# Kernel tuning notes

Measured on AMD Instinct MI355X. Metric: run time of the kernel, lower is better.

The kernel has to match this reference:

```python
import jax, jax.numpy as jnp
import numpy as np
import math

B, N, D, L, H, FF, T = 8, 256, 384, 6, 8, 1536, 4
Dh = D // H  # 48, divisible by 6 for 3D rotary
N_M1 = T + 1 + 2 * N  # learn tokens + state + hand + head
S = 2 * N_M1


def rotary_pe_3d(x, coords):
    # x: [B,H,S,Dh], coords: [B,S,3]. Split head dim into 3 axis chunks,
    # apply standard RoPE per axis using the continuous coordinate as position.
    dh = x.shape[-1]
    d = dh // 3
    half = d // 2
    inv_freq = 1.0 / (10000.0 ** (jnp.arange(half, dtype=x.dtype) / half))
    outs = []
    for a in range(3):
        xa = x[..., a * d:(a + 1) * d]
        ang = coords[..., a][:, None, :, None] * inv_freq  # [B,1,S,half]
        c, s = jnp.cos(ang), jnp.sin(ang)
        x1, x2 = xa[..., :half], xa[..., half:]
        outs.append(jnp.concatenate([x1 * c - x2 * s, x1 * s + x2 * c], axis=-1))
    return jnp.concatenate(outs, axis=-1)


def layernorm(x, g, b):
    m = jnp.mean(x, axis=-1, keepdims=True)
    v = jnp.var(x, axis=-1, keepdims=True)
    return (x - m) * jax.lax.rsqrt(v + 1e-5) * g + b


def transformer_layer(src, coords_src, mask, Wq, bq, Wk, bk, Wv, bv, Wo, bo, W1, b1, W2, b2, g1, be1, g2, be2):
    Bsz, Ss, _ = src.shape
    q = jnp.einsum('bsd,od->bso', src, Wq) + bq
    k = jnp.einsum('bsd,od->bso', src, Wk) + bk
    v = jnp.einsum('bsd,od->bso', src, Wv) + bv
    q = q.reshape(Bsz, Ss, H, Dh).transpose(0, 2, 1, 3)
    k = k.reshape(Bsz, Ss, H, Dh).transpose(0, 2, 1, 3)
    v = v.reshape(Bsz, Ss, H, Dh).transpose(0, 2, 1, 3)
    q = rotary_pe_3d(q, coords_src)
    k = rotary_pe_3d(k, coords_src)
    scores = jnp.einsum('bhqd,bhkd->bhqk', q, k) / math.sqrt(Dh)
    scores = jnp.where(mask[None, None, :, :], -jnp.inf, scores)
    attn = jnp.einsum('bhqk,bhkd->bhqd', jax.nn.softmax(scores, axis=-1), v)
    attn = attn.transpose(0, 2, 1, 3).reshape(Bsz, Ss, D)
    attn = jnp.einsum('bsd,od->bso', attn, Wo) + bo
    src2 = layernorm(src + attn, g1, be1)
    ff = jnp.einsum('bsf,of->bso', jax.nn.gelu(jnp.einsum('bsd,fd->bsf', src2, W1) + b1, approximate=False), W2) + b2
    return layernorm(src2 + ff, g2, be2)


def setup_inputs() -> dict:
    key = jax.random.key(0)
    ks = jax.random.split(key, 32)
    rnd = lambda i, shape, scale=1.0: (jax.random.normal(ks[i], shape, dtype=jnp.float32) * scale)
    inp = {
        'hand_token_t': rnd(0, (B, N, D)),
        'head_token_t': rnd(1, (B, N, D)),
        'hand_token_m1': rnd(2, (B, N, D)),
        'head_token_m1': rnd(3, (B, N, D)),
        'coords_hand_t': rnd(4, (B, N, 3)),
        'coords_head_t': rnd(5, (B, N, 3)),
        'coords_hand_m1': rnd(6, (B, N, 3)),
        'coords_head_m1': rnd(7, (B, N, 3)),
        'state_t': rnd(8, (B, D)),
        'state_m1': rnd(9, (B, D)),
        'trans_head_t': rnd(10, (B, 3)),
        'trans_head_m1': rnd(11, (B, 3)),
        'tokens_m1': rnd(12, (1, T, D), 0.02),
        'tokens_t': rnd(13, (1, T, D), 0.02),
        'Wq': rnd(14, (L, D, D), 0.02), 'bq': jnp.zeros((L, D), jnp.float32),
        'Wk': rnd(15, (L, D, D), 0.02), 'bk': jnp.zeros((L, D), jnp.float32),
        'Wv': rnd(16, (L, D, D), 0.02), 'bv': jnp.zeros((L, D), jnp.float32),
        'Wo': rnd(17, (L, D, D), 0.02), 'bo': jnp.zeros((L, D), jnp.float32),
        'W1': rnd(18, (L, FF, D), 0.02), 'b1': jnp.zeros((L, FF), jnp.float32),
        'W2': rnd(19, (L, D, FF), 0.02), 'b2': jnp.zeros((L, D), jnp.float32),
        'g1': jnp.ones((L, D), jnp.float32), 'be1': jnp.zeros((L, D), jnp.float32),
        'g2': jnp.ones((L, D), jnp.float32), 'be2': jnp.zeros((L, D), jnp.float32),
    }
    return inp


def reference(hand_token_t, head_token_t, hand_token_m1, head_token_m1,
              coords_hand_t, coords_head_t, coords_hand_m1, coords_head_m1,
              state_t, state_m1, trans_head_t, trans_head_m1,
              tokens_m1, tokens_t, Wq, bq, Wk, bk, Wv, bv, Wo, bo,
              W1, b1, W2, b2, g1, be1, g2, be2):
    # Build token sequence: [state_m1, hand_m1, head_m1, learn_m1, state_t, hand_t, head_t, learn_t]
    tok_m1 = jnp.broadcast_to(tokens_m1, (B, T, D))
    tok_t = jnp.broadcast_to(tokens_t, (B, T, D))
    coord_m1 = jnp.broadcast_to(trans_head_m1[:, None, :], (B, T, 3))
    coord_t = jnp.broadcast_to(trans_head_t[:, None, :], (B, T, 3))
    src = jnp.concatenate([
        state_m1[:, None, :], hand_token_m1, head_token_m1, tok_m1,
        state_t[:, None, :], hand_token_t, head_token_t, tok_t], axis=1)
    coords_src = jnp.concatenate([
        trans_head_m1[:, None, :], coords_hand_m1, coords_head_m1, coord_m1,
        trans_head_t[:, None, :], coords_hand_t, coords_head_t, coord_t], axis=1)
    # block-causal mask: m1 block cannot attend to t block
    mask = jnp.zeros((S, S), dtype=bool).at[:N_M1, N_M1:].set(True)
    for i in range(L):
        src = transformer_layer(src, coords_src, mask,
                                Wq[i], bq[i], Wk[i], bk[i], Wv[i], bv[i], Wo[i], bo[i],
                                W1[i], b1[i], W2[i], b2[i], g1[i], be1[i], g2[i], be2[i])
    return src[:, -T:, :]
```

## Files before the change

### kernel.cpp

```cpp
#include <hip/hip_runtime.h>
#include <hip/hip_bf16.h>
#include <math.h>

#define BB 8
#define NN 256
#define DD 384
#define LL 6
#define HH 8
#define FFD 1536
#define TT 4
#define DH 48
#define NM1 517
#define SS 1034
#define SSP 1088
#define MROWS (BB*SS)
#define NQKV 1152
#define QSCALE2 (0.14433756729740643f * 1.4426950408889634f)

typedef unsigned short u16;
typedef unsigned int u32;
typedef short bf8 __attribute__((ext_vector_type(8)));
typedef float f32x4 __attribute__((ext_vector_type(4)));

__device__ __forceinline__ u16 f2bf(float f) {
  __hip_bfloat16 h = __float2bfloat16(f);
  return *reinterpret_cast<u16*>(&h);
}
__device__ __forceinline__ float bf2f(u16 u) {
  __hip_bfloat16 h;
  *reinterpret_cast<u16*>(&h) = u;
  return __bfloat162float(h);
}
__device__ __forceinline__ float max3f(float a, float b, float c) {
  return fmaxf(fmaxf(a, b), c);
}
__device__ __forceinline__ void async16(void* lds, const void* g) {
  __builtin_amdgcn_global_load_lds(
      (const __attribute__((address_space(1))) unsigned int*)g,
      (__attribute__((address_space(3))) unsigned int*)lds, 16, 0, 0);
}

__global__ void build_src(const float* __restrict__ hand_t, const float* __restrict__ head_t,
                          const float* __restrict__ hand_m1, const float* __restrict__ head_m1,
                          const float* __restrict__ state_t, const float* __restrict__ state_m1,
                          const float* __restrict__ tok_m1, const float* __restrict__ tok_t,
                          float* __restrict__ src, u16* __restrict__ srcb) {
  int idx = blockIdx.x * 256 + threadIdx.x;
  if (idx >= BB * SS * DD) return;
  int d = idx % DD;
  int bs = idx / DD;
  int s = bs % SS;
  int b = bs / SS;
  float val;
  if (s == 0)               val = state_m1[b * DD + d];
  else if (s <= NN)         val = hand_m1[((size_t)(b * NN + (s - 1))) * DD + d];
  else if (s <= 2 * NN)     val = head_m1[((size_t)(b * NN + (s - 1 - NN))) * DD + d];
  else if (s <= 2 * NN + TT) val = tok_m1[(s - (2 * NN + 1)) * DD + d];
  else if (s == NM1)        val = state_t[b * DD + d];
  else if (s <= NM1 + NN)   val = hand_t[((size_t)(b * NN + (s - NM1 - 1))) * DD + d];
  else if (s <= NM1 + 2 * NN) val = head_t[((size_t)(b * NN + (s - NM1 - 1 - NN))) * DD + d];
  else                      val = tok_t[(s - (NM1 + 2 * NN + 1)) * DD + d];
  src[idx] = val;
  srcb[idx] = f2bf(val);
}

__global__ void build_coords(const float* __restrict__ c_hand_t, const float* __restrict__ c_head_t,
                             const float* __restrict__ c_hand_m1, const float* __restrict__ c_head_m1,
                             const float* __restrict__ tr_t, const float* __restrict__ tr_m1,
                             float* __restrict__ coords) {
  int idx = blockIdx.x * 256 + threadIdx.x;
  if (idx >= BB * SS * 3) return;
  int a = idx % 3;
  int bs = idx / 3;
  int s = bs % SS;
  int b = bs / SS;
  float val;
  if (s == 0)               val = tr_m1[b * 3 + a];
  else if (s <= NN)         val = c_hand_m1[(b * NN + (s - 1)) * 3 + a];
  else if (s <= 2 * NN)     val = c_head_m1[(b * NN + (s - 1 - NN)) * 3 + a];
  else if (s <= 2 * NN + TT) val = tr_m1[b * 3 + a];
  else if (s == NM1)        val = tr_t[b * 3 + a];
  else if (s <= NM1 + NN)   val = c_hand_t[(b * NN + (s - NM1 - 1)) * 3 + a];
  else if (s <= NM1 + 2 * NN) val = c_head_t[(b * NN + (s - NM1 - 1 - NN)) * 3 + a];
  else                      val = tr_t[b * 3 + a];
  coords[idx] = val;
}

__global__ void build_trig(const float* __restrict__ coords, float2* __restrict__ trig) {
  int idx = blockIdx.x * 256 + threadIdx.x;
  if (idx >= BB * SS * 24) return;
  int i = idx & 7;
  int axis = (idx >> 3) % 3;
  int bs = idx / 24;
  float cv = coords[bs * 3 + axis];
  float inv = expf(-(float)i * 1.1512925464970229f);
  float ang = cv * inv;
  trig[idx] = make_float2(cosf(ang), sinf(ang));
}

__global__ void cvt_bf(const float* __restrict__ in, u16* __restrict__ out, int n4) {
  int idx = blockIdx.x * 256 + threadIdx.x;
  if (idx >= n4) return;
  float4 v = reinterpret_cast<const float4*>(in)[idx];
  short4 o;
  o.x = (short)f2bf(v.x); o.y = (short)f2bf(v.y);
  o.z = (short)f2bf(v.z); o.w = (short)f2bf(v.w);
  reinterpret_cast<short4*>(out)[idx] = o;
}

__global__ void pack_qkv(const float* __restrict__ Wq, const float* __restrict__ Wk,
                         const float* __restrict__ Wv, u16* __restrict__ wqkv) {
  int idx = blockIdx.x * 256 + threadIdx.x;
  const int TOTAL = LL * NQKV * 96;
  if (idx >= TOTAL) return;
  int k4 = idx % 96;
  int n = (idx / 96) % NQKV;
  int l = idx / (96 * NQKV);
  int sel = n / 384, nn = n - sel * 384;
  const float* W = (sel == 0) ? Wq : ((sel == 1) ? Wk : Wv);
  float4 v = *reinterpret_cast<const float4*>(W + ((size_t)l * 384 + nn) * 384 + k4 * 4);
  short4 o;
  o.x = (short)f2bf(v.x); o.y = (short)f2bf(v.y);
  o.z = (short)f2bf(v.z); o.w = (short)f2bf(v.w);
  *reinterpret_cast<short4*>(wqkv + ((size_t)(l * NQKV + n) * 384 + k4 * 4)) = o;
}

__global__ void pack_bqkv(const float* __restrict__ bq, const float* __restrict__ bk,
                          const float* __restrict__ bv, float* __restrict__ bqkv) {
  int idx = blockIdx.x * 256 + threadIdx.x;
  if (idx >= LL * NQKV) return;
  int n = idx % NQKV, l = idx / NQKV;
  int sel = n / 384, nn = n - sel * 384;
  const float* Bp = (sel == 0) ? bq : ((sel == 1) ? bk : bv);
  bqkv[idx] = Bp[l * 384 + nn];
}

__global__ void pad_vt(u16* __restrict__ vt) {
  int idx = blockIdx.x * 256 + threadIdx.x;
  const int PADW = SSP - SS;
  if (idx >= 64 * DH * PADW) return;
  int c = idx % PADW;
  int rd = idx / PADW;
  vt[(size_t)rd * SSP + SS + c] = 0;
}

__global__ void pad_qk(u16* __restrict__ qh, u16* __restrict__ kh) {
  int idx = blockIdx.x * 256 + threadIdx.x;
  if (idx >= 64 * SS * 16) return;
  int c = idx & 15;
  int row = idx >> 4;
  qh[(size_t)row * 64 + 48 + c] = 0;
  kh[(size_t)row * 64 + 48 + c] = 0;
}

template <int EPI, int OUT>
__global__ __launch_bounds__(512) void gemm_as(
    const u16* __restrict__ Ab, const u16* __restrict__ Wb,
    const float* __restrict__ bias, const float2* __restrict__ trig,
    const float* __restrict__ Rf,
    float* __restrict__ Cf, u16* __restrict__ Cb,
    u16* __restrict__ Ck, u16* __restrict__ Cv,
    int M, int N, int K) {
  constexpr int BUFSZ = 24576;
  __shared__ __align__(16) char sm[2 * BUFSZ];
  const int tid = threadIdx.x;

  const int nxt = N >> 6;
  const int Mt = (M + 127) >> 7;
  const int gL = blockIdx.x;
  const int x8 = gL & 7, jj = gL >> 3;
  const int mt_ = x8 * 9 + jj / nxt;
  if (mt_ >= Mt) return;
  const int bm = mt_ << 7, bn = (jj % nxt) << 6;

  const int lid = tid & 63, w = tid >> 6;
  const int wm = w >> 1, wn = w & 1;
  const int l15 = lid & 15, lg = lid >> 4;
  const int lr = lid >> 3, lu = lid & 7;
  const int swz = lu ^ lr;
  f32x4 acc[2][2] = {};

  auto stage = [&](int bsel, int k0) {
    char* base = sm + bsel * BUFSZ;
#pragma unroll
    for (int q = 0; q < 2; ++q) {
      int row = w * 16 + q * 8 + lr;
      int grow = bm + row; if (grow >= M) grow = M - 1;
      async16(base + w * 2048 + q * 1024, Ab + (size_t)grow * K + k0 + (swz << 3));
    }
    async16(base + 16384 + w * 1024, Wb + (size_t)(bn + w * 8 + lr) * K + k0 + (swz << 3));
  };

  stage(0, 0);
  int bs = 0;

  for (int k0 = 0; k0 < K; k0 += 64) {
    if (k0 + 64 < K) {
      stage(bs ^ 1, k0 + 64);
      asm volatile("s_waitcnt vmcnt(3)" ::: "memory");
    } else {
      asm volatile("s_waitcnt vmcnt(0)" ::: "memory");
    }
    __builtin_amdgcn_s_barrier();
    const char* base = sm + bs * BUFSZ;
    bf8 a[2][2], bfr[2][2];
#pragma unroll
    for (int kf = 0; kf < 2; ++kf) {
#pragma unroll
      for (int mt = 0; mt < 2; ++mt) {
        int row = wm * 32 + mt * 16 + l15;
        int off = ((row << 7) + (kf << 6) + (lg << 4)) ^ ((row & 7) << 4);
        a[kf][mt] = *reinterpret_cast<const bf8*>(base + off);
      }
#pragma unroll
      for (int nt = 0; nt < 2; ++nt) {
        int row = wn * 32 + nt * 16 + l15;
        int off = 16384 + (((row << 7) + (kf << 6) + (lg << 4)) ^ ((row & 7) << 4));
        bfr[kf][nt] = *reinterpret_cast<const bf8*>(base + off);
      }
    }
#pragma unroll
    for (int kf = 0; kf < 2; ++kf)
#pragma unroll
      for (int mt = 0; mt < 2; ++mt)
#pragma unroll
        for (int nt = 0; nt < 2; ++nt)
          acc[mt][nt] = __builtin_amdgcn_mfma_f32_16x16x32_bf16(a[kf][mt], bfr[kf][nt], acc[mt][nt], 0, 0, 0);
    asm volatile("s_waitcnt lgkmcnt(0)" ::: "memory");
    __builtin_amdgcn_s_barrier();
    bs ^= 1;
  }

  if constexpr (OUT != 2) {
#pragma unroll
    for (int nt = 0; nt < 2; ++nt) {
      const int n = bn + wn * 32 + nt * 16 + l15;
      const float bsv = bias[n];
#pragma unroll
      for (int mt = 0; mt < 2; ++mt) {
        const int m0 = bm + wm * 32 + mt * 16 + lg * 4;
#pragma unroll
        for (int r = 0; r < 4; ++r) {
          int m = m0 + r;
          if (m >= M) continue;
          float v = acc[mt][nt][r] + bsv;
          if (EPI == 1) v = 0.5f * v * (1.0f + erff(v * 0.70710678118654752f));
          if (OUT == 0) Cf[(size_t)m * N + n] = v + Rf[(size_t)m * N + n];
          else          Cb[(size_t)m * N + n] = f2bf(v);
        }
      }
    }
  } else {
    float* tile = (float*)sm;
#pragma unroll
    for (int nt = 0; nt < 2; ++nt) {
      const int nl = wn * 32 + nt * 16 + l15;
      const float bsv = bias[bn + nl];
#pragma unroll
      for (int mt = 0; mt < 2; ++mt) {
#pragma unroll
        for (int r = 0; r < 4; ++r) {
          int ml = wm * 32 + mt * 16 + lg * 4 + r;
          tile[ml * 65 + nl] = acc[mt][nt][r] + bsv;
        }
      }
    }
    __syncthreads();
    const int bnm = bn % 384;
    const int sel = bn / 384;
    if (sel < 2) {
      u16* Cqk = (sel == 0) ? Cb : Ck;
      const int d = lid;
      const int nn_ = bnm + d;
      const int hdiv = nn_ / 48, hrem = nn_ - hdiv * 48;
      const int axis = hrem >> 4, ii = hrem & 7;
      const bool hi = (hrem & 8) != 0;
      for (int si = 0; si < 16; ++si) {
        int row = w * 16 + si;
        int m = bm + row;
        if (m >= M) break;
        int bI = m / SS, s = m - bI * SS;
        float v = tile[row * 65 + d];
        float p = tile[row * 65 + (d ^ 8)];
        float2 t = trig[(size_t)(bI * SS + s) * 24 + axis * 8 + ii];
        float outv = hi ? (p * t.y + v * t.x) : (v * t.x - p * t.y);
        if (sel == 0) outv *= QSCALE2;
        Cqk[((size_t)(bI * HH + hdiv) * SS + s) * 64 + hrem] = f2bf(outv);
      }
    } else {
      const int srow = tid & 127, dq = tid >> 7;
      const int m = bm + srow;
      if (m < M) {
        int bI = m / SS, s = m - bI * SS;
        for (int di = 0; di < 16; ++di) {
          int d = dq * 16 + di;
          int nn_ = bnm + d;
          int hdiv = nn_ / 48, hrem = nn_ - hdiv * 48;
          Cv[((size_t)(bI * HH + hdiv) * DH + hrem) * SSP + s] = f2bf(tile[srow * 65 + d]);
        }
      }
    }
  }
}

__global__ __launch_bounds__(512) void attn_mfma(const u16* __restrict__ qh,
                                                 const u16* __restrict__ kh,
                                                 const u16* __restrict__ vt,
                                                 u16* __restrict__ outb) {
  __shared__ __align__(16) char sm[32768];
  const int tid = threadIdx.x;
  const int lid = tid & 63, w = tid >> 6;
  const int l15 = lid & 15, lg = lid >> 4;
  const int lr = lid >> 3, lu = lid & 7;
  const int swz8 = (lu ^ lr) << 3;

  const int f = blockIdx.x;
  const int low = f & 7, j = f >> 3;
  const int gi = j / 9, qp = j - gi * 9;
  const int g = gi * 8 + low;
  const int h = g & 7, b = g >> 3;
  const int qblk = (qp < 5) ? (4 + qp) : (qp - 5);
  const int bh = b * HH + h;
  const int q0w = qblk * 128 + w * 16;
  const u16* kbase = kh + (size_t)bh * SS * 64;
  const u16* vbase = vt + (size_t)bh * DH * SSP;

  bf8 qf[2];
  {
    int row = q0w + l15; if (row >= SS) row = SS - 1;
    const u16* qp_ = qh + ((size_t)bh * SS + row) * 64;
    qf[0] = *reinterpret_cast<const bf8*>(qp_ + lg * 8);
    qf[1] = *reinterpret_cast<const bf8*>(qp_ + 32 + lg * 8);
  }
  const int qrow = q0w + l15;

  float m_q = -1e30f, l_q = 0.f;
  f32x4 accO[3] = {};

  const int nch = (qblk < 4) ? 9 : 17;

  auto stage = [&](int bsel, int c) {
    const int j0 = c * 64;
    char* kb = sm + bsel * 16384;
    char* vb = kb + 8192;
    {
      int s = w * 8 + lr;
      int jt_ = s >> 4, lgs = (s >> 2) & 3, rr = s & 3;
      int p = ((jt_ >> 1) << 5) + (lgs << 3) + ((jt_ & 1) << 2) + rr;
      int jrow = j0 + p; if (jrow >= SS) jrow = SS - 1;
      async16(kb + w * 1024, kbase + (size_t)jrow * 64 + swz8);
    }
    {
      int vrow = w * 8 + lr; if (vrow >= DH) vrow = DH - 1;
      async16(vb + w * 1024, vbase + (size_t)vrow * SSP + j0 + swz8);
    }
  };

  stage(0, 0);
  __syncthreads();
  int bsel = 0;

  for (int c = 0; c < nch; ++c) {
    if (c + 1 < nch) {
      stage(bsel ^ 1, c + 1);
      asm volatile("s_waitcnt vmcnt(2)" ::: "memory");
    } else {
      asm volatile("s_waitcnt vmcnt(0)" ::: "memory");
    }
    __builtin_amdgcn_s_barrier();
    const int j0 = c * 64;
    const char* kb = sm + bsel * 16384;
    const char* vb = kb + 8192;

    f32x4 sv[4];
    __builtin_amdgcn_s_setprio(1);
#pragma unroll
    for (int jt = 0; jt < 4; ++jt) {
      int row = jt * 16 + l15;
      int off0 = ((row << 7) + (lg << 4)) ^ ((row & 7) << 4);
      int off1 = ((row << 7) + 64 + (lg << 4)) ^ ((row & 7) << 4);
      bf8 kb0 = *reinterpret_cast<const bf8*>(kb + off0);
      bf8 kb1 = *reinterpret_cast<const bf8*>(kb + off1);
      f32x4 z = {};
      z = __builtin_amdgcn_mfma_f32_16x16x32_bf16(kb0, qf[0], z, 0, 0, 0);
      z = __builtin_amdgcn_mfma_f32_16x16x32_bf16(kb1, qf[1], z, 0, 0, 0);
      sv[jt] = z;
    }
    __builtin_amdgcn_s_setprio(0);

    const bool domask = (c == 16) | ((q0w < NM1) & (c >= 8));
    if (domask) {
#pragma unroll
      for (int jt = 0; jt < 4; ++jt)
#pragma unroll
        for (int r = 0; r < 4; ++r) {
          int kabs = j0 + ((jt >> 1) << 5) + (lg << 3) + ((jt & 1) << 2) + r;
          if (kabs >= SS || (qrow < NM1 && kabs >= NM1)) sv[jt][r] = -1e30f;
        }
    }

    float mx = max3f(sv[0][0], sv[0][1], sv[0][2]);
    mx = max3f(mx, sv[0][3], sv[1][0]);
    mx = max3f(mx, sv[1][1], sv[1][2]);
    mx = max3f(mx, sv[1][3], sv[2][0]);
    mx = max3f(mx, sv[2][1], sv[2][2]);
    mx = max3f(mx, sv[2][3], sv[3][0]);
    mx = max3f(mx, sv[3][1], sv[3][2]);
    mx = fmaxf(mx, sv[3][3]);
    mx = fmaxf(mx, __shfl_xor(mx, 16));
    mx = fmaxf(mx, __shfl_xor(mx, 32));

    const bool skip = __all(mx <= m_q);
    const float mn = skip ? m_q : fmaxf(m_q, mx);

    float pv[4][4];
    float ps = 0.f;
#pragma unroll
    for (int jt = 0; jt < 4; ++jt)
#pragma unroll
      for (int r = 0; r < 4; ++r) {
        float p = __builtin_amdgcn_exp2f(sv[jt][r] - mn);
        pv[jt][r] = p;
        ps += p;
      }
    ps += __shfl_xor(ps, 16);
    ps += __shfl_xor(ps, 32);

    if (!skip) {
      float alpha = __builtin_amdgcn_exp2f(m_q - mn);
      l_q = l_q * alpha + ps;
      m_q = mn;
      const int lg4 = lg * 4;
      float a0 = __shfl(alpha, lg4);
      float a1 = __shfl(alpha, lg4 + 1);
      float a2 = __shfl(alpha, lg4 + 2);
      float a3 = __shfl(alpha, lg4 + 3);
#pragma unroll
      for (int dt = 0; dt < 3; ++dt) {
        accO[dt][0] *= a0; accO[dt][1] *= a1;
        accO[dt][2] *= a2; accO[dt][3] *= a3;
      }
    } else {
      l_q += ps;
    }

    bf8 pa[2];
#pragma unroll
    for (int jc = 0; jc < 2; ++jc) {
      u32 w0 = (u32)f2bf(pv[jc * 2][0])     | ((u32)f2bf(pv[jc * 2][1]) << 16);
      u32 w1 = (u32)f2bf(pv[jc * 2][2])     | ((u32)f2bf(pv[jc * 2][3]) << 16);
      u32 w2 = (u32)f2bf(pv[jc * 2 + 1][0]) | ((u32)f2bf(pv[jc * 2 + 1][1]) << 16);
      u32 w3 = (u32)f2bf(pv[jc * 2 + 1][2]) | ((u32)f2bf(pv[jc * 2 + 1][3]) << 16);
      uint4 t = make_uint4(w0, w1, w2, w3);
      pa[jc] = *reinterpret_cast<bf8*>(&t);
    }

    __builtin_amdgcn_s_setprio(1);
#pragma unroll
    for (int dt = 0; dt < 3; ++dt) {
      int row = dt * 16 + l15;
#pragma unroll
      for (int jc = 0; jc < 2; ++jc) {
        int off = ((row << 7) + (jc << 6) + (lg << 4)) ^ ((row & 7) << 4);
        bf8 vb8 = *reinterpret_cast<const bf8*>(vb + off);
        accO[dt] = __builtin_amdgcn_mfma_f32_16x16x32_bf16(pa[jc], vb8, accO[dt], 0, 0, 0);
      }
    }
    __builtin_amdgcn_s_setprio(0);
    asm volatile("s_waitcnt lgkmcnt(0)" ::: "memory");
    __builtin_amdgcn_s_barrier();
    bsel ^= 1;
  }

  float linv = 1.0f / l_q;
  const int lg4 = lg * 4;
  float il[4];
#pragma unroll
  for (int r = 0; r < 4; ++r) il[r] = __shfl(linv, lg4 + r);
#pragma unroll
  for (int r = 0; r < 4; ++r) {
    int q = q0w + lg4 + r;
    if (q >= SS) continue;
#pragma unroll
    for (int dt = 0; dt < 3; ++dt) {
      int d = dt * 16 + l15;
      outb[((size_t)(b * SS + q)) * DD + h * DH + d] = f2bf(accO[dt][r] * il[r]);
    }
  }
}

__global__ __launch_bounds__(512) void add_ln(const float* __restrict__ a,
                                              const float* __restrict__ g,
                                              const float* __restrict__ be,
                                              float* __restrict__ out,
                                              u16* __restrict__ outb) {
  __shared__ float p1[4][2], p2[4][2];
  const int rl = threadIdx.x >> 7;
  const int t = threadIdx.x & 127;
  const int row = blockIdx.x * 4 + rl;
  const size_t base = (size_t)row * DD;
  float x0 = a[base + t];
  float x1 = a[base + t + 128];
  float x2 = a[base + t + 256];
  float s = x0 + x1 + x2;
#pragma unroll
  for (int off = 32; off; off >>= 1) s += __shfl_xor(s, off);
  if ((t & 63) == 0) p1[rl][t >> 6] = s;
  __syncthreads();
  float mean = (p1[rl][0] + p1[rl][1]) * (1.0f / 384.0f);
  float d0 = x0 - mean, d1 = x1 - mean, d2 = x2 - mean;
  float vsum = d0 * d0 + d1 * d1 + d2 * d2;
#pragma unroll
  for (int off = 32; off; off >>= 1) vsum += __shfl_xor(vsum, off);
  if ((t & 63) == 0) p2[rl][t >> 6] = vsum;
  __syncthreads();
  float var = (p2[rl][0] + p2[rl][1]) * (1.0f / 384.0f);
  float rs = rsqrtf(var + 1e-5f);
  float o0 = d0 * rs * g[t]       + be[t];
  float o1 = d1 * rs * g[t + 128] + be[t + 128];
  float o2 = d2 * rs * g[t + 256] + be[t + 256];
  out[base + t] = o0;        outb[base + t] = f2bf(o0);
  out[base + t + 128] = o1;  outb[base + t + 128] = f2bf(o1);
  out[base + t + 256] = o2;  outb[base + t + 256] = f2bf(o2);
}

__global__ void copy_out(const float* __restrict__ src, float* __restrict__ out) {
  int idx = blockIdx.x * 256 + threadIdx.x;
  if (idx >= BB * TT * DD) return;
  int d = idx % DD;
  int bt = idx / DD;
  int t = bt % TT;
  int b = bt / TT;
  out[idx] = src[((size_t)b * SS + (SS - TT) + t) * DD + d];
}

extern "C" void kernel_launch(void* const* d_in, const int* in_sizes, int n_in,
                              void* d_out, int out_size, void* d_ws, size_t ws_size,
                              hipStream_t stream) {
  const float* hand_t    = (const float*)d_in[0];
  const float* head_t    = (const float*)d_in[1];
  const float* hand_m1   = (const float*)d_in[2];
  const float* head_m1   = (const float*)d_in[3];
  const float* c_hand_t  = (const float*)d_in[4];
  const float* c_head_t  = (const float*)d_in[5];
  const float* c_hand_m1 = (const float*)d_in[6];
  const float* c_head_m1 = (const float*)d_in[7];
  const float* state_t   = (const float*)d_in[8];
  const float* state_m1  = (const float*)d_in[9];
  const float* tr_t      = (const float*)d_in[10];
  const float* tr_m1     = (const float*)d_in[11];
  const float* tok_m1    = (const float*)d_in[12];
  const float* tok_t     = (const float*)d_in[13];
  const float* Wq = (const float*)d_in[14];
  const float* bq = (const float*)d_in[15];
  const float* Wk = (const float*)d_in[16];
  const float* bk = (const float*)d_in[17];
  const float* Wv = (const float*)d_in[18];
  const float* bv = (const float*)d_in[19];
  const float* Wo = (const float*)d_in[20];
  const float* bo = (const float*)d_in[21];
  const float* W1 = (const float*)d_in[22];
  const float* b1 = (const float*)d_in[23];
  const float* W2 = (const float*)d_in[24];
  const float* b2 = (const float*)d_in[25];
  const float* g1 = (const float*)d_in[26];
  const float* be1 = (const float*)d_in[27];
  const float* g2 = (const float*)d_in[28];
  const float* be2 = (const float*)d_in[29];

  const size_t SRC_N = (size_t)BB * SS * DD;
  float* src    = (float*)d_ws;
  float* src2   = src + SRC_N;
  float* bufB   = src2 + SRC_N;
  float* coords = bufB + SRC_N;
  float* bqkv   = coords + (size_t)BB * SS * 3;
  float2* trig  = (float2*)(bqkv + (size_t)LL * NQKV);
  u16* srcb  = (u16*)(trig + (size_t)BB * SS * 24);
  u16* src2b = srcb + SRC_N;
  u16* attnb = src2b + SRC_N;
  u16* qh  = attnb + SRC_N;
  const size_t QH_N = (size_t)BB * HH * SS * 64;
  u16* khb = qh + QH_N;
  u16* vtb = khb + QH_N;
  u16* hbf = vtb + (size_t)64 * DH * SSP;
  u16* wqkv_b = hbf + (size_t)MROWS * FFD;
  const size_t WD = (size_t)LL * DD * DD;
  const size_t WF = (size_t)LL * FFD * DD;
  u16* wo_bf = wqkv_b + (size_t)LL * NQKV * 384;
  u16* w1_bf = wo_bf + WD;
  u16* w2_bf = w1_bf + WF;

  const int M = MROWS;
  dim3 blk(256);
  dim3 blk512(512);

  build_src<<<(BB * SS * DD + 255) / 256, blk, 0, stream>>>(
      hand_t, head_t, hand_m1, head_m1, state_t, state_m1, tok_m1, tok_t, src, srcb);
  build_coords<<<(BB * SS * 3 + 255) / 256, blk, 0, stream>>>(
      c_hand_t, c_head_t, c_hand_m1, c_head_m1, tr_t, tr_m1, coords);
  build_trig<<<(BB * SS * 24 + 255) / 256, blk, 0, stream>>>(coords, trig);
  pack_qkv<<<(LL * NQKV * 96 + 255) / 256, blk, 0, stream>>>(Wq, Wk, Wv, wqkv_b);
  pack_bqkv<<<(LL * NQKV + 255) / 256, blk, 0, stream>>>(bq, bk, bv, bqkv);
  cvt_bf<<<(int)(WD / 4 + 255) / 256, blk, 0, stream>>>(Wo, wo_bf, (int)(WD / 4));
  cvt_bf<<<(int)(WF / 4 + 255) / 256, blk, 0, stream>>>(W1, w1_bf, (int)(WF / 4));
  cvt_bf<<<(int)(WF / 4 + 255) / 256, blk, 0, stream>>>(W2, w2_bf, (int)(WF / 4));
  pad_vt<<<(64 * DH * (SSP - SS) + 255) / 256, blk, 0, stream>>>(vtb);
  pad_qk<<<(64 * SS * 16 + 255) / 256, blk, 0, stream>>>(qh, khb);

  dim3 gqkv(18 * 72);
  dim3 gwo(6 * 72);
  dim3 gf1(24 * 72);
  dim3 gf2(6 * 72);
  dim3 gattn(9 * 8 * 8);

  for (int l = 0; l < LL; ++l) {
    const u16* Wqkv_l = wqkv_b + (size_t)l * NQKV * 384;
    const u16* Wo_l = wo_bf + (size_t)l * DD * DD;
    const u16* W1_l = w1_bf + (size_t)l * FFD * DD;
    const u16* W2_l = w2_bf + (size_t)l * DD * FFD;

    gemm_as<0, 2><<<gqkv, blk512, 0, stream>>>(srcb, Wqkv_l, bqkv + l * NQKV, trig,
                                               nullptr, nullptr, qh, khb, vtb, M, NQKV, DD);
    attn_mfma<<<gattn, blk512, 0, stream>>>(qh, khb, vtb, attnb);
    gemm_as<0, 0><<<gwo, blk512, 0, stream>>>(attnb, Wo_l, bo + l * DD, nullptr,
                                              src, bufB, nullptr, nullptr, nullptr, M, DD, DD);
    add_ln<<<M / 4, blk512, 0, stream>>>(bufB, g1 + l * DD, be1 + l * DD, src2, src2b);
    gemm_as<1, 1><<<gf1, blk512, 0, stream>>>(src2b, W1_l, b1 + l * FFD, nullptr,
                                              nullptr, nullptr, hbf, nullptr, nullptr, M, FFD, DD);
    gemm_as<0, 0><<<gf2, blk512, 0, stream>>>(hbf, W2_l, b2 + l * DD, nullptr,
                                              src2, bufB, nullptr, nullptr, nullptr, M, DD, FFD);
    add_ln<<<M / 4, blk512, 0, stream>>>(bufB, g2 + l * DD, be2 + l * DD, src, srcb);
  }
  copy_out<<<(BB * TT * DD + 255) / 256, blk, 0, stream>>>(src, (float*)d_out);
}
```

Baseline: 906.6 us.

## Split long attention query blocks across KV halves, templatize GEMM dims, warp-per-row layernorm

Query blocks in the t half, which attend over 17 KV chunks, are now split into two work items of 9 and 8 chunks. Each writes unnormalized partial outputs plus its max and sum to scratch, and a new merge kernel combines them. This balances per-block work against the 9-chunk m1 blocks and raises the attention grid size, at the cost of an extra launch and scratch traffic through the src2/bufB buffers. Separately, GEMM M/N/K become compile-time template constants with an unrolled K loop, and layernorm now uses one wavefront per row with no shared-memory reductions or barriers.

```diff
diff --git a/kernel.cpp b/kernel.cpp
--- a/kernel.cpp
+++ b/kernel.cpp
@@ -153,20 +153,20 @@
   kh[(size_t)row * 64 + 48 + c] = 0;
 }
 
-template <int EPI, int OUT>
+template <int EPI, int OUT, int Nc, int Kc>
 __global__ __launch_bounds__(512) void gemm_as(
     const u16* __restrict__ Ab, const u16* __restrict__ Wb,
     const float* __restrict__ bias, const float2* __restrict__ trig,
     const float* __restrict__ Rf,
     float* __restrict__ Cf, u16* __restrict__ Cb,
-    u16* __restrict__ Ck, u16* __restrict__ Cv,
-    int M, int N, int K) {
+    u16* __restrict__ Ck, u16* __restrict__ Cv) {
   constexpr int BUFSZ = 24576;
+  constexpr int M = MROWS;
+  constexpr int nxt = Nc >> 6;
+  constexpr int Mt = (M + 127) >> 7;
   __shared__ __align__(16) char sm[2 * BUFSZ];
   const int tid = threadIdx.x;
 
-  const int nxt = N >> 6;
-  const int Mt = (M + 127) >> 7;
   const int gL = blockIdx.x;
   const int x8 = gL & 7, jj = gL >> 3;
   const int mt_ = x8 * 9 + jj / nxt;
@@ -186,16 +186,17 @@
     for (int q = 0; q < 2; ++q) {
       int row = w * 16 + q * 8 + lr;
       int grow = bm + row; if (grow >= M) grow = M - 1;
-      async16(base + w * 2048 + q * 1024, Ab + (size_t)grow * K + k0 + (swz << 3));
-    }
-    async16(base + 16384 + w * 1024, Wb + (size_t)(bn + w * 8 + lr) * K + k0 + (swz << 3));
+      async16(base + w * 2048 + q * 1024, Ab + (size_t)grow * Kc + k0 + (swz << 3));
+    }
+    async16(base + 16384 + w * 1024, Wb + (size_t)(bn + w * 8 + lr) * Kc + k0 + (swz << 3));
   };
 
   stage(0, 0);
   int bs = 0;
 
-  for (int k0 = 0; k0 < K; k0 += 64) {
-    if (k0 + 64 < K) {
+#pragma unroll
+  for (int k0 = 0; k0 < Kc; k0 += 64) {
+    if (k0 + 64 < Kc) {
       stage(bs ^ 1, k0 + 64);
       asm volatile("s_waitcnt vmcnt(3)" ::: "memory");
     } else {
@@ -245,8 +246,8 @@
           if (m >= M) continue;
           float v = acc[mt][nt][r] + bsv;
           if (EPI == 1) v = 0.5f * v * (1.0f + erff(v * 0.70710678118654752f));
-          if (OUT == 0) Cf[(size_t)m * N + n] = v + Rf[(size_t)m * N + n];
-          else          Cb[(size_t)m * N + n] = f2bf(v);
+          if (OUT == 0) Cf[(size_t)m * Nc + n] = v + Rf[(size_t)m * Nc + n];
+          else          Cb[(size_t)m * Nc + n] = f2bf(v);
         }
       }
     }
@@ -306,7 +307,9 @@
 __global__ __launch_bounds__(512) void attn_mfma(const u16* __restrict__ qh,
                                                  const u16* __restrict__ kh,
                                                  const u16* __restrict__ vt,
-                                                 u16* __restrict__ outb) {
+                                                 u16* __restrict__ outb,
+                                                 float* __restrict__ scr0,
+                                                 float* __restrict__ scr1) {
   __shared__ __align__(16) char sm[32768];
   const int tid = threadIdx.x;
   const int lid = tid & 63, w = tid >> 6;
@@ -316,10 +319,12 @@
 
   const int f = blockIdx.x;
   const int low = f & 7, j = f >> 3;
-  const int gi = j / 9, qp = j - gi * 9;
+  const int gi = j / 14, it = j - gi * 14;
   const int g = gi * 8 + low;
   const int h = g & 7, b = g >> 3;
-  const int qblk = (qp < 5) ? (4 + qp) : (qp - 5);
+  int qblk, c0, c1, part;
+  if (it < 10) { qblk = 4 + (it >> 1); part = it & 1; c0 = part ? 9 : 0; c1 = part ? 17 : 9; }
+  else         { qblk = it - 10;       part = -1;     c0 = 0;            c1 = 9; }
   const int bh = b * HH + h;
   const int q0w = qblk * 128 + w * 16;
   const u16* kbase = kh + (size_t)bh * SS * 64;
@@ -336,8 +341,6 @@
 
   float m_q = -1e30f, l_q = 0.f;
   f32x4 accO[3] = {};
-
-  const int nch = (qblk < 4) ? 9 : 17;
 
   auto stage = [&](int bsel, int c) {
     const int j0 = c * 64;
@@ -356,12 +359,12 @@
     }
   };
 
-  stage(0, 0);
+  stage(0, c0);
   __syncthreads();
   int bsel = 0;
 
-  for (int c = 0; c < nch; ++c) {
-    if (c + 1 < nch) {
+  for (int c = c0; c < c1; ++c) {
+    if (c + 1 < c1) {
       stage(bsel ^ 1, c + 1);
       asm volatile("s_waitcnt vmcnt(2)" ::: "memory");
     } else {
@@ -472,21 +475,61 @@
     bsel ^= 1;
   }
 
-  float linv = 1.0f / l_q;
   const int lg4 = lg * 4;
-  float il[4];
-#pragma unroll
-  for (int r = 0; r < 4; ++r) il[r] = __shfl(linv, lg4 + r);
-#pragma unroll
-  for (int r = 0; r < 4; ++r) {
-    int q = q0w + lg4 + r;
-    if (q >= SS) continue;
-#pragma unroll
-    for (int dt = 0; dt < 3; ++dt) {
-      int d = dt * 16 + l15;
-      outb[((size_t)(b * SS + q)) * DD + h * DH + d] = f2bf(accO[dt][r] * il[r]);
+  if (part < 0) {
+    float linv = 1.0f / l_q;
+    float il[4];
+#pragma unroll
+    for (int r = 0; r < 4; ++r) il[r] = __shfl(linv, lg4 + r);
+#pragma unroll
+    for (int r = 0; r < 4; ++r) {
+      int q = q0w + lg4 + r;
+      if (q >= SS) continue;
+#pragma unroll
+      for (int dt = 0; dt < 3; ++dt) {
+        int d = dt * 16 + l15;
+        outb[((size_t)(b * SS + q)) * DD + h * DH + d] = f2bf(accO[dt][r] * il[r]);
+      }
+    }
+  } else {
+    float* pb = (part == 0) ? scr0 : scr1;
+    const size_t base2 = (size_t)(bh * 5 + (qblk - 4)) * (128 * 50);
+#pragma unroll
+    for (int r = 0; r < 4; ++r) {
+      int qloc = w * 16 + lg4 + r;
+#pragma unroll
+      for (int dt = 0; dt < 3; ++dt)
+        pb[base2 + (size_t)qloc * 50 + dt * 16 + l15] = accO[dt][r];
+    }
+    if (lg == 0) {
+      int qloc = w * 16 + l15;
+      pb[base2 + (size_t)qloc * 50 + 48] = m_q;
+      pb[base2 + (size_t)qloc * 50 + 49] = l_q;
     }
   }
+}
+
+__global__ void attn_merge(const float* __restrict__ s1, const float* __restrict__ s2,
+                           u16* __restrict__ outb) {
+  int idx = blockIdx.x * 256 + threadIdx.x;
+  if (idx >= 64 * 5 * 128 * 48) return;
+  int d = idx % 48;
+  int row = idx / 48;
+  int qloc = row & 127;
+  int slot = row >> 7;
+  int bh = slot / 5, qi = slot - bh * 5;
+  int q = (4 + qi) * 128 + qloc;
+  if (q >= SS) return;
+  size_t o1 = (size_t)slot * (128 * 50) + qloc * 50;
+  float m1 = s1[o1 + 48], l1 = s1[o1 + 49];
+  float m2 = s2[o1 + 48], l2 = s2[o1 + 49];
+  float m = fmaxf(m1, m2);
+  float a1 = __builtin_amdgcn_exp2f(m1 - m);
+  float a2 = __builtin_amdgcn_exp2f(m2 - m);
+  float l = l1 * a1 + l2 * a2;
+  float o = (s1[o1 + d] * a1 + s2[o1 + d] * a2) / l;
+  int b = bh >> 3, h = bh & 7;
+  outb[((size_t)(b * SS + q)) * DD + h * DH + d] = f2bf(o);
 }
 
 __global__ __launch_bounds__(512) void add_ln(const float* __restrict__ a,
@@ -494,34 +537,29 @@
                                               const float* __restrict__ be,
                                               float* __restrict__ out,
                                               u16* __restrict__ outb) {
-  __shared__ float p1[4][2], p2[4][2];
-  const int rl = threadIdx.x >> 7;
-  const int t = threadIdx.x & 127;
-  const int row = blockIdx.x * 4 + rl;
+  const int w = threadIdx.x >> 6, lane = threadIdx.x & 63;
+  const int row = blockIdx.x * 8 + w;
   const size_t base = (size_t)row * DD;
-  float x0 = a[base + t];
-  float x1 = a[base + t + 128];
-  float x2 = a[base + t + 256];
-  float s = x0 + x1 + x2;
+  float x[6];
+#pragma unroll
+  for (int jj = 0; jj < 6; ++jj) x[jj] = a[base + lane + 64 * jj];
+  float s = x[0] + x[1] + x[2] + x[3] + x[4] + x[5];
 #pragma unroll
   for (int off = 32; off; off >>= 1) s += __shfl_xor(s, off);
-  if ((t & 63) == 0) p1[rl][t >> 6] = s;
-  __syncthreads();
-  float mean = (p1[rl][0] + p1[rl][1]) * (1.0f / 384.0f);
-  float d0 = x0 - mean, d1 = x1 - mean, d2 = x2 - mean;
-  float vsum = d0 * d0 + d1 * d1 + d2 * d2;
-#pragma unroll
-  for (int off = 32; off; off >>= 1) vsum += __shfl_xor(vsum, off);
-  if ((t & 63) == 0) p2[rl][t >> 6] = vsum;
-  __syncthreads();
-  float var = (p2[rl][0] + p2[rl][1]) * (1.0f / 384.0f);
-  float rs = rsqrtf(var + 1e-5f);
-  float o0 = d0 * rs * g[t]       + be[t];
-  float o1 = d1 * rs * g[t + 128] + be[t + 128];
-  float o2 = d2 * rs * g[t + 256] + be[t + 256];
-  out[base + t] = o0;        outb[base + t] = f2bf(o0);
-  out[base + t + 128] = o1;  outb[base + t + 128] = f2bf(o1);
-  out[base + t + 256] = o2;  outb[base + t + 256] = f2bf(o2);
+  float mean = s * (1.0f / 384.0f);
+  float dv[6], vs = 0.f;
+#pragma unroll
+  for (int jj = 0; jj < 6; ++jj) { dv[jj] = x[jj] - mean; vs += dv[jj] * dv[jj]; }
+#pragma unroll
+  for (int off = 32; off; off >>= 1) vs += __shfl_xor(vs, off);
+  float rs = rsqrtf(vs * (1.0f / 384.0f) + 1e-5f);
+#pragma unroll
+  for (int jj = 0; jj < 6; ++jj) {
+    int c = lane + 64 * jj;
+    float o = dv[jj] * rs * g[c] + be[c];
+    out[base + c] = o;
+    outb[base + c] = f2bf(o);
+  }
 }
 
 __global__ void copy_out(const float* __restrict__ src, float* __restrict__ out) {
@@ -590,7 +628,6 @@
   u16* w1_bf = wo_bf + WD;
   u16* w2_bf = w1_bf + WF;
 
-  const int M = MROWS;
   dim3 blk(256);
   dim3 blk512(512);
 
@@ -611,7 +648,8 @@
   dim3 gwo(6 * 72);
   dim3 gf1(24 * 72);
   dim3 gf2(6 * 72);
-  dim3 gattn(9 * 8 * 8);
+  dim3 gattn(14 * 8 * 8);
+  dim3 gmrg((64 * 5 * 128 * 48 + 255) / 256);
 
   for (int l = 0; l < LL; ++l) {
     const u16* Wqkv_l = wqkv_b + (size_t)l * NQKV * 384;
@@ -619,17 +657,18 @@
     const u16* W1_l = w1_bf + (size_t)l * FFD * DD;
     const u16* W2_l = w2_bf + (size_t)l * DD * FFD;
 
-    gemm_as<0, 2><<<gqkv, blk512, 0, stream>>>(srcb, Wqkv_l, bqkv + l * NQKV, trig,
-                                               nullptr, nullptr, qh, khb, vtb, M, NQKV, DD);
-    attn_mfma<<<gattn, blk512, 0, stream>>>(qh, khb, vtb, attnb);
-    gemm_as<0, 0><<<gwo, blk512, 0, stream>>>(attnb, Wo_l, bo + l * DD, nullptr,
-                                              src, bufB, nullptr, nullptr, nullptr, M, DD, DD);
-    add_ln<<<M / 4, blk512, 0, stream>>>(bufB, g1 + l * DD, be1 + l * DD, src2, src2b);
-    gemm_as<1, 1><<<gf1, blk512, 0, stream>>>(src2b, W1_l, b1 + l * FFD, nullptr,
-                                              nullptr, nullptr, hbf, nullptr, nullptr, M, FFD, DD);
-    gemm_as<0, 0><<<gf2, blk512, 0, stream>>>(hbf, W2_l, b2 + l * DD, nullptr,
-                                              src2, bufB, nullptr, nullptr, nullptr, M, DD, FFD);
-    add_ln<<<M / 4, blk512, 0, stream>>>(bufB, g2 + l * DD, be2 + l * DD, src, srcb);
+    gemm_as<0, 2, NQKV, DD><<<gqkv, blk512, 0, stream>>>(
+        srcb, Wqkv_l, bqkv + l * NQKV, trig, nullptr, nullptr, qh, khb, vtb);
+    attn_mfma<<<gattn, blk512, 0, stream>>>(qh, khb, vtb, attnb, src2, bufB);
+    attn_merge<<<gmrg, blk, 0, stream>>>(src2, bufB, attnb);
+    gemm_as<0, 0, DD, DD><<<gwo, blk512, 0, stream>>>(
+        attnb, Wo_l, bo + l * DD, nullptr, src, bufB, nullptr, nullptr, nullptr);
+    add_ln<<<MROWS / 8, blk512, 0, stream>>>(bufB, g1 + l * DD, be1 + l * DD, src2, src2b);
+    gemm_as<1, 1, FFD, DD><<<gf1, blk512, 0, stream>>>(
+        src2b, W1_l, b1 + l * FFD, nullptr, nullptr, nullptr, hbf, nullptr, nullptr);
+    gemm_as<0, 0, DD, FFD><<<gf2, blk512, 0, stream>>>(
+        hbf, W2_l, b2 + l * DD, nullptr, src2, bufB, nullptr, nullptr, nullptr);
+    add_ln<<<MROWS / 8, blk512, 0, stream>>>(bufB, g2 + l * DD, be2 + l * DD, src, srcb);
   }
   copy_out<<<(BB * TT * DD + 255) / 256, blk, 0, stream>>>(src, (float*)d_out);
 }
```

Result: no change. 906.2 us (-0.0%).
